# Optimization experiments

Measured on AMD Instinct MI355X. Metric: run time of the kernel, lower is better.

## Reference

```python
import jax, jax.numpy as jnp
import numpy as np
import math

B, NPG, DEG = 100, 500, 12          # graphs, nodes/graph, avg degree
F_IN, H, C = 128, 128, 10
RATIO = 0.5
N = B * NPG
E = N * DEG
K1 = math.ceil(NPG * RATIO)          # 250
K2 = math.ceil(K1 * RATIO)           # 125
K3 = math.ceil(K2 * RATIO)           # 63


def _lin(k, i, o):
    return jax.random.uniform(k, (i, o), jnp.float32, -1.0, 1.0) / np.sqrt(i).astype(np.float32)


def setup_inputs() -> dict:
    key = jax.random.key(0)
    ks = jax.random.split(key, 16)
    x = jax.random.normal(ks[0], (N, F_IN), jnp.float32)
    off = (jnp.arange(B, dtype=jnp.int32) * NPG)[:, None]
    src = (jax.random.randint(ks[1], (B, NPG * DEG), 0, NPG, jnp.int32) + off).reshape(-1)
    dst = (jax.random.randint(ks[2], (B, NPG * DEG), 0, NPG, jnp.int32) + off).reshape(-1)
    edge_index = jnp.stack([src, dst])
    return {
        'x': x, 'edge_index': edge_index,
        'Wl1': _lin(ks[3], F_IN, H), 'bl1': jnp.zeros((H,), jnp.float32), 'Wr1': _lin(ks[4], F_IN, H),
        'Wl2': _lin(ks[5], H, H), 'bl2': jnp.zeros((H,), jnp.float32), 'Wr2': _lin(ks[6], H, H),
        'Wl3': _lin(ks[7], H, H), 'bl3': jnp.zeros((H,), jnp.float32), 'Wr3': _lin(ks[8], H, H),
        'pw1': jax.random.normal(ks[9], (H,), jnp.float32),
        'pw2': jax.random.normal(ks[10], (H,), jnp.float32),
        'pw3': jax.random.normal(ks[11], (H,), jnp.float32),
        'W1': _lin(ks[12], 2 * H, H), 'b1': jnp.zeros((H,), jnp.float32),
        'W2': _lin(ks[13], H, H // 2), 'b2': jnp.zeros((H // 2,), jnp.float32),
        'W3': _lin(ks[14], H // 2, C), 'b3': jnp.zeros((C,), jnp.float32),
    }


def sage_conv(x, src, dst, emask, Wl, bl, Wr, n_nodes):
    # PyG SAGEConv: out_i = lin_l(mean_{j->i} x_j) + lin_r(x_i)
    msg = x[src] * emask[:, None]                                   # [E, d]
    agg = jax.ops.segment_sum(msg, dst, num_segments=n_nodes)
    cnt = jax.ops.segment_sum(emask, dst, num_segments=n_nodes)
    mean = agg / jnp.maximum(cnt, 1.0)[:, None]
    return mean @ Wl + bl + x @ Wr


def topk_pool(x, w, src, dst, emask, n_per, k):
    # TopKPooling: score = tanh(x.w/||w||); keep top-k nodes per graph; x_kept *= score
    score = jnp.tanh((x @ w) / jnp.linalg.norm(w))                  # [B*n_per]
    topv, topi = jax.lax.top_k(score.reshape(B, n_per), k)          # [B, k]
    perm = (topi + (jnp.arange(B, dtype=jnp.int32) * n_per)[:, None]).reshape(-1)
    x_new = x[perm] * topv.reshape(-1)[:, None]                     # [B*k, d]
    mapping = jnp.full((B * n_per,), -1, jnp.int32).at[perm].set(jnp.arange(B * k, dtype=jnp.int32))
    ns, nd = mapping[src], mapping[dst]
    emask_new = emask * ((ns >= 0) & (nd >= 0)).astype(emask.dtype)
    return x_new, jnp.maximum(ns, 0), jnp.maximum(nd, 0), emask_new


def readout(x, k):
    # global_max_pool || global_mean_pool (all graphs have exactly k nodes)
    xr = x.reshape(B, k, H)
    return jnp.concatenate([xr.max(axis=1), xr.mean(axis=1)], axis=1)  # [B, 2H]


def reference(x, edge_index, Wl1, bl1, Wr1, Wl2, bl2, Wr2, Wl3, bl3, Wr3,
              pw1, pw2, pw3, W1, b1, W2, b2, W3, b3):
    src, dst = edge_index[0], edge_index[1]
    emask = jnp.ones((E,), jnp.float32)
    h = jax.nn.relu(sage_conv(x, src, dst, emask, Wl1, bl1, Wr1, N))
    h, src, dst, emask = topk_pool(h, pw1, src, dst, emask, NPG, K1)
    x1 = readout(h, K1)
    h = jax.nn.relu(sage_conv(h, src, dst, emask, Wl2, bl2, Wr2, B * K1))
    h, src, dst, emask = topk_pool(h, pw2, src, dst, emask, K1, K2)
    x2 = readout(h, K2)
    h = jax.nn.relu(sage_conv(h, src, dst, emask, Wl3, bl3, Wr3, B * K2))
    h, src, dst, emask = topk_pool(h, pw3, src, dst, emask, K2, K3)
    x3 = readout(h, K3)
    z = x1 + x2 + x3
    z = jax.nn.relu(z @ W1 + b1)   # dropout is identity in eval mode
    z = jax.nn.relu(z @ W2 + b2)
    return jax.nn.log_softmax(z @ W3 + b3, axis=1)   # pool_loss == 0 for TopKPool
```

## Files before the change

kernel.cpp:

```cpp
#include <hip/hip_runtime.h>
#include <math.h>

#define BG    100
#define NPG   500
#define FD    128
#define EE    600000
#define EPG   6000
#define NN    50000
#define K1    250
#define K2    125
#define K3    63
#define CAP   64

typedef short v8s __attribute__((ext_vector_type(8)));
typedef float v4f __attribute__((ext_vector_type(4)));

__device__ __forceinline__ int swz(int p, int N) {
    int j = p & 7, i = p >> 3;
    int chunk = N >> 3, rem = N & 7;
    int mj = j < rem ? j : rem;
    return j * chunk + mj + i;
}

__device__ __forceinline__ unsigned short f2bf(float f) {
    unsigned int u = __float_as_uint(f);
    unsigned int r = (u + 0x7FFFu + ((u >> 16) & 1u)) >> 16;
    return (unsigned short)r;
}
__device__ __forceinline__ float bf2f(unsigned short b) {
    return __uint_as_float(((unsigned int)b) << 16);
}

__global__ __launch_bounds__(1024) void prep_fill_kernel(
        const int* __restrict__ ei, int* __restrict__ deg, int* __restrict__ col,
        const float* __restrict__ Wl1, const float* __restrict__ Wr1,
        const float* __restrict__ Wl2, const float* __restrict__ Wr2,
        const float* __restrict__ Wl3, const float* __restrict__ Wr3,
        unsigned short* __restrict__ wt_hi, unsigned short* __restrict__ wt_lo) {
    __shared__ int lcnt[NPG];
    int tid = threadIdx.x;
    if (blockIdx.x < BG) {
        int b = swz(blockIdx.x, BG);
        for (int i = tid; i < NPG; i += 1024) lcnt[i] = 0;
        __syncthreads();
        for (int e0 = tid; e0 < EPG; e0 += 1024) {
            int e = b * EPG + e0;
            int d = ei[EE + e];
            int pos = atomicAdd(&lcnt[d - b * NPG], 1);
            if (pos < CAP) col[(long long)d * CAP + pos] = ei[e];
        }
        __syncthreads();
        for (int i = tid; i < NPG; i += 1024) deg[b * NPG + i] = lcnt[i];
    } else {
        int id = (blockIdx.x - BG) * 1024 + tid;
        if (id >= 3 * 256 * 128) return;
        int layer = id >> 15, rem = id & 32767;
        int k = rem >> 7, n = rem & 127;
        const float* Wl = layer == 0 ? Wl1 : (layer == 1 ? Wl2 : Wl3);
        const float* Wr = layer == 0 ? Wr1 : (layer == 1 ? Wr2 : Wr3);
        float w = (k < 128) ? Wl[k * 128 + n] : Wr[(k - 128) * 128 + n];
        unsigned short hi = f2bf(w);
        unsigned short lo = f2bf(w - bf2f(hi));
        long long o = (long long)layer * 32768 + n * 256 + k;
        wt_hi[o] = hi;
        wt_lo[o] = lo;
    }
}

__global__ void gather_agg_kernel(const int* __restrict__ deg, const int* __restrict__ col,
                                  const float* __restrict__ x, float* __restrict__ mean,
                                  int n, int NB) {
    int g = swz(blockIdx.x, NB) * 256 + threadIdx.x;
    int node = g >> 5, sub = g & 31;
    if (node >= n) return;
    int d = deg[node]; if (d > CAP) d = CAP;
    const int* cp = col + (long long)node * CAP;
    float ax = 0.0f, ay = 0.0f, az = 0.0f, aw = 0.0f;
    int j = 0;
    for (; j + 4 <= d; j += 4) {
        int s0 = cp[j], s1 = cp[j + 1], s2 = cp[j + 2], s3 = cp[j + 3];
        float4 v0 = ((const float4*)(x + (long long)s0 * FD))[sub];
        float4 v1 = ((const float4*)(x + (long long)s1 * FD))[sub];
        float4 v2 = ((const float4*)(x + (long long)s2 * FD))[sub];
        float4 v3 = ((const float4*)(x + (long long)s3 * FD))[sub];
        ax += v0.x; ay += v0.y; az += v0.z; aw += v0.w;
        ax += v1.x; ay += v1.y; az += v1.z; aw += v1.w;
        ax += v2.x; ay += v2.y; az += v2.z; aw += v2.w;
        ax += v3.x; ay += v3.y; az += v3.z; aw += v3.w;
    }
    for (; j < d; ++j) {
        float4 v = ((const float4*)(x + (long long)cp[j] * FD))[sub];
        ax += v.x; ay += v.y; az += v.z; aw += v.w;
    }
    float inv = 1.0f / fmaxf((float)d, 1.0f);
    float4 o; o.x = ax * inv; o.y = ay * inv; o.z = az * inv; o.w = aw * inv;
    ((float4*)(mean + (long long)node * FD))[sub] = o;
}

__global__ __launch_bounds__(256) void sage_gemm_mfma_kernel(
        const float* __restrict__ mean, const float* __restrict__ x,
        const unsigned short* __restrict__ wt_hi, const unsigned short* __restrict__ wt_lo,
        const float* __restrict__ bl, const float* __restrict__ pw,
        float* __restrict__ hout, float* __restrict__ score, int M, int NB) {
    __shared__ unsigned short Bh[128 * 40], Bl[128 * 40];
    __shared__ float spart[64 * 16];
    __shared__ float snrmp[16];
    int tid  = threadIdx.x;
    int wave = tid >> 6, lane = tid & 63;
    int quad = lane >> 4, l15 = lane & 15;
    int row0 = swz(blockIdx.x, NB) * 64;

    v4f acc[8];
#pragma unroll
    for (int t = 0; t < 8; t++) acc[t] = (v4f){0.f, 0.f, 0.f, 0.f};

    if (tid < 16) {
        float s = 0.f;
#pragma unroll
        for (int t = 0; t < 8; t++) { float p = pw[t * 16 + tid]; s += p * p; }
        snrmp[tid] = s;
    }

    int growA = row0 + 16 * wave + l15; if (growA > M - 1) growA = M - 1;
    int brow = tid >> 1;
    int bk   = (tid & 1) * 16;

    for (int kt = 0; kt < 8; ++kt) {
        const float* Ab = (kt < 4) ? mean : x;
        const float* ap = Ab + (long long)growA * FD + ((kt < 4) ? kt : kt - 4) * 32 + quad * 8;
        float4 v0 = *(const float4*)(ap);
        float4 v1 = *(const float4*)(ap + 4);
        {
            int klog = kt * 32;
            const uint4* sh = (const uint4*)(wt_hi + (long long)brow * 256 + klog + bk);
            const uint4* sl = (const uint4*)(wt_lo + (long long)brow * 256 + klog + bk);
            uint4 vh0 = sh[0], vh1 = sh[1];
            uint4 vl0 = sl[0], vl1 = sl[1];
            *(uint4*)&Bh[brow * 40 + bk]     = vh0;
            *(uint4*)&Bh[brow * 40 + bk + 8] = vh1;
            *(uint4*)&Bl[brow * 40 + bk]     = vl0;
            *(uint4*)&Bl[brow * 40 + bk + 8] = vl1;
        }
        float f[8] = {v0.x, v0.y, v0.z, v0.w, v1.x, v1.y, v1.z, v1.w};
        v8s a_h, a_l;
#pragma unroll
        for (int q = 0; q < 8; q++) {
            unsigned short hb = f2bf(f[q]);
            a_h[q] = (short)hb;
            a_l[q] = (short)f2bf(f[q] - bf2f(hb));
        }
        __syncthreads();
#pragma unroll
        for (int t = 0; t < 8; t++) {
            v8s b_h = *(const v8s*)&Bh[(t * 16 + l15) * 40 + quad * 8];
            v8s b_l = *(const v8s*)&Bl[(t * 16 + l15) * 40 + quad * 8];
            acc[t] = __builtin_amdgcn_mfma_f32_16x16x32_bf16(a_l, b_h, acc[t], 0, 0, 0);
            acc[t] = __builtin_amdgcn_mfma_f32_16x16x32_bf16(a_h, b_l, acc[t], 0, 0, 0);
            acc[t] = __builtin_amdgcn_mfma_f32_16x16x32_bf16(a_h, b_h, acc[t], 0, 0, 0);
        }
        __syncthreads();
    }

    int rbase = row0 + 16 * wave + quad * 4;
    float part[4] = {0.f, 0.f, 0.f, 0.f};
#pragma unroll
    for (int t = 0; t < 8; t++) {
        int colc = t * 16 + l15;
        float blv = bl[colc];
        float pwv = pw[colc];
#pragma unroll
        for (int reg = 0; reg < 4; reg++) {
            float h = fmaxf(acc[t][reg] + blv, 0.0f);
            part[reg] += h * pwv;
            int grow = rbase + reg;
            if (grow < M) hout[(long long)grow * FD + colc] = h;
        }
    }
#pragma unroll
    for (int reg = 0; reg < 4; reg++)
        spart[(16 * wave + quad * 4 + reg) * 16 + l15] = part[reg];
    __syncthreads();
    if (tid < 64) {
        int grow = row0 + tid;
        if (grow < M) {
            float dot = 0.0f;
#pragma unroll
            for (int i = 0; i < 16; i++) dot += spart[tid * 16 + i];
            float nr = 0.0f;
#pragma unroll
            for (int i = 0; i < 16; i++) nr += snrmp[i];
            score[grow] = tanhf(dot / sqrtf(nr));
        }
    }
}

__global__ __launch_bounds__(1024) void topk_tail_kernel(
        const float* __restrict__ score, const float* __restrict__ hout,
        int n_per, int k, int SN,
        float* __restrict__ xp,
        const int* __restrict__ esrc, const int* __restrict__ edst,
        const float* __restrict__ em_in,
        int* __restrict__ src_out, int* __restrict__ dst_out, float* __restrict__ em_out,
        int* __restrict__ next_deg, int* __restrict__ next_col,
        float* __restrict__ z, int mode,
        const float* __restrict__ W1, const float* __restrict__ b1,
        const float* __restrict__ W2, const float* __restrict__ b2,
        const float* __restrict__ W3, const float* __restrict__ b3,
        float* __restrict__ out) {
    __shared__ float skey[512];
    __shared__ int   sidx[512];
    __shared__ unsigned long long spk[512];
    __shared__ int   lmap[512];
    __shared__ int   lcnt[512];
    __shared__ float pmax[1024];
    __shared__ float psum[1024];
    __shared__ float zs[256], t1[128], t2[64], t3[16];
    int b = swz(blockIdx.x, BG), tid = threadIdx.x;

    for (int i = tid; i < SN; i += 1024) { lmap[i] = -1; lcnt[i] = 0; }

    unsigned long long P = 0ULL;
    if (tid < SN) {
        float keyv; unsigned int idx;
        if (tid < n_per) { keyv = score[b * n_per + tid]; idx = (unsigned int)tid; }
        else             { keyv = -INFINITY;              idx = 0x7fffffffu; }
        unsigned int u = __float_as_uint(keyv);
        u = (u & 0x80000000u) ? ~u : (u | 0x80000000u);
        P = ((unsigned long long)u << 32) | (unsigned long long)(~idx);
    }

    for (int ks = 2; ks <= SN; ks <<= 1) {
        for (int j = ks >> 1; j > 0; j >>= 1) {
            unsigned long long Q;
            if (j >= 64) {
                __syncthreads();
                if (tid < SN) spk[tid] = P;
                __syncthreads();
                Q = (tid < SN) ? spk[tid ^ j] : 0ULL;
            } else {
                Q = __shfl_xor(P, j, 64);
            }
            if (tid < SN) {
                bool keepmax = (((tid & ks) == 0) == ((tid & j) == 0));
                if (keepmax == (Q > P)) P = Q;
            }
        }
    }
    if (tid < SN) {
        unsigned int u  = (unsigned int)(P >> 32);
        unsigned int fb = (u & 0x80000000u) ? (u & 0x7fffffffu) : ~u;
        int iv = (int)(~(unsigned int)P);
        skey[tid] = __uint_as_float(fb);
        sidx[tid] = iv;
        if (tid < k) lmap[iv] = tid;
    }
    __syncthreads();

    if (esrc) {
        int nbase = b * n_per, kbase = b * k;
        for (int e0 = tid; e0 < EPG; e0 += 1024) {
            int e = b * EPG + e0;
            bool alive = em_in ? (em_in[e] != 0.0f) : true;
            if (alive) {
                int ls = lmap[esrc[e] - nbase];
                int ld = lmap[edst[e] - nbase];
                bool keep = (ls >= 0) && (ld >= 0);
                if (keep) {
                    int pos = atomicAdd(&lcnt[ld], 1);
                    if (pos < CAP) next_col[(long long)(kbase + ld) * CAP + pos] = kbase + ls;
                }
                if (em_out) {
                    em_out[e]  = keep ? 1.0f : 0.0f;
                    src_out[e] = keep ? kbase + ls : 0;
                    dst_out[e] = keep ? kbase + ld : 0;
                }
            } else if (em_out) {
                em_out[e] = 0.0f; src_out[e] = 0; dst_out[e] = 0;
            }
        }
        __syncthreads();
        for (int i = tid; i < k; i += 1024) next_deg[b * k + i] = lcnt[i];
    }

    int c = tid & 127, s = tid >> 7;
    float mx = -INFINITY, sm = 0.0f;
    {
        int r = s;
        long long hbase = (long long)b * n_per * FD + c;
        long long xbase = (long long)b * k * FD + c;
        for (; r + 24 < k; r += 32) {
            int i0 = sidx[r], i1 = sidx[r + 8], i2 = sidx[r + 16], i3 = sidx[r + 24];
            float k0 = skey[r], k1 = skey[r + 8], k2 = skey[r + 16], k3 = skey[r + 24];
            float v0 = hout[hbase + (long long)i0 * FD] * k0;
            float v1 = hout[hbase + (long long)i1 * FD] * k1;
            float v2 = hout[hbase + (long long)i2 * FD] * k2;
            float v3 = hout[hbase + (long long)i3 * FD] * k3;
            xp[xbase + (long long)(r)      * FD] = v0;
            xp[xbase + (long long)(r + 8)  * FD] = v1;
            xp[xbase + (long long)(r + 16) * FD] = v2;
            xp[xbase + (long long)(r + 24) * FD] = v3;
            mx = fmaxf(mx, v0); sm += v0;
            mx = fmaxf(mx, v1); sm += v1;
            mx = fmaxf(mx, v2); sm += v2;
            mx = fmaxf(mx, v3); sm += v3;
        }
        for (; r < k; r += 8) {
            float v = hout[hbase + (long long)sidx[r] * FD] * skey[r];
            xp[xbase + (long long)r * FD] = v;
            mx = fmaxf(mx, v); sm += v;
        }
    }
    pmax[tid] = mx; psum[tid] = sm;
    __syncthreads();
    if (tid < 128) {
        float m = -INFINITY, su = 0.0f;
#pragma unroll
        for (int i = 0; i < 8; i++) {
            m = fmaxf(m, pmax[i * 128 + tid]);
            su += psum[i * 128 + tid];
        }
        float mean = su / (float)k;
        if (mode == 0)      { z[b * 256 + tid] = m;  z[b * 256 + 128 + tid] = mean;  }
        else if (mode == 1) { z[b * 256 + tid] += m; z[b * 256 + 128 + tid] += mean; }
        else {
            zs[tid]       = z[b * 256 + tid] + m;
            zs[128 + tid] = z[b * 256 + 128 + tid] + mean;
        }
    }
    if (mode == 2) {
        __syncthreads();
        if (tid < 128) {
            float a = b1[tid];
            for (int kk = 0; kk < 256; kk++) a += zs[kk] * W1[kk * 128 + tid];
            t1[tid] = fmaxf(a, 0.0f);
        }
        __syncthreads();
        if (tid < 64) {
            float a = b2[tid];
            for (int kk = 0; kk < 128; kk++) a += t1[kk] * W2[kk * 64 + tid];
            t2[tid] = fmaxf(a, 0.0f);
        }
        __syncthreads();
        if (tid < 10) {
            float a = b3[tid];
            for (int kk = 0; kk < 64; kk++) a += t2[kk] * W3[kk * 10 + tid];
            t3[tid] = a;
        }
        __syncthreads();
        if (tid == 0) {
            float m = -INFINITY;
            for (int i = 0; i < 10; i++) m = fmaxf(m, t3[i]);
            float su = 0.0f;
            for (int i = 0; i < 10; i++) su += expf(t3[i] - m);
            float ls = logf(su);
            for (int i = 0; i < 10; i++) out[b * 10 + i] = t3[i] - m - ls;
        }
    }
}

extern "C" void kernel_launch(void* const* d_in, const int* in_sizes, int n_in,
                              void* d_out, int out_size, void* d_ws, size_t ws_size,
                              hipStream_t stream) {
    (void)in_sizes; (void)n_in; (void)out_size; (void)ws_size;
    const float* x   = (const float*)d_in[0];
    const int*   ei  = (const int*)d_in[1];
    const float* Wl1 = (const float*)d_in[2];
    const float* bl1 = (const float*)d_in[3];
    const float* Wr1 = (const float*)d_in[4];
    const float* Wl2 = (const float*)d_in[5];
    const float* bl2 = (const float*)d_in[6];
    const float* Wr2 = (const float*)d_in[7];
    const float* Wl3 = (const float*)d_in[8];
    const float* bl3 = (const float*)d_in[9];
    const float* Wr3 = (const float*)d_in[10];
    const float* pw1 = (const float*)d_in[11];
    const float* pw2 = (const float*)d_in[12];
    const float* pw3 = (const float*)d_in[13];
    const float* W1  = (const float*)d_in[14];
    const float* b1  = (const float*)d_in[15];
    const float* W2  = (const float*)d_in[16];
    const float* b2  = (const float*)d_in[17];
    const float* W3  = (const float*)d_in[18];
    const float* b3  = (const float*)d_in[19];
    float* out = (float*)d_out;

    char* ws = (char*)d_ws;
    size_t off = 0;
    auto alloc = [&](size_t bytes) {
        char* p = ws + off;
        off = (off + bytes + 255) & ~(size_t)255;
        return p;
    };
    float* mean  = (float*)alloc((size_t)NN * FD * 4);
    float* hout  = (float*)alloc((size_t)NN * FD * 4);
    float* xp    = (float*)alloc((size_t)BG * K1 * FD * 4);
    float* sc    = (float*)alloc((size_t)NN * 4);
    int*   srcb  = (int*)  alloc((size_t)EE * 4);
    int*   dstb  = (int*)  alloc((size_t)EE * 4);
    float* emb   = (float*)alloc((size_t)EE * 4);
    int*   deg   = (int*)  alloc((size_t)NN * 4);
    int*   colb  = (int*)  alloc((size_t)NN * CAP * 4);
    float* z     = (float*)alloc((size_t)BG * 256 * 4);
    unsigned short* wt_hi = (unsigned short*)alloc((size_t)3 * 32768 * 2);
    unsigned short* wt_lo = (unsigned short*)alloc((size_t)3 * 32768 * 2);

    prep_fill_kernel<<<BG + 96, 1024, 0, stream>>>(ei, deg, colb,
                                                   Wl1, Wr1, Wl2, Wr2, Wl3, Wr3, wt_hi, wt_lo);

    {
        int nb = (NN * 32 + 255) / 256;
        gather_agg_kernel<<<nb, 256, 0, stream>>>(deg, colb, x, mean, NN, nb);
    }
    {
        int nb = (NN + 63) / 64;
        sage_gemm_mfma_kernel<<<nb, 256, 0, stream>>>(mean, x, wt_hi, wt_lo,
                                                      bl1, pw1, hout, sc, NN, nb);
    }
    topk_tail_kernel<<<BG, 1024, 0, stream>>>(sc, hout, NPG, K1, 512, xp,
                                              ei, ei + EE, (const float*)0,
                                              srcb, dstb, emb, deg, colb,
                                              z, 0, W1, b1, W2, b2, W3, b3, out);

    const int N2 = BG * K1;
    {
        int nb = (N2 * 32 + 255) / 256;
        gather_agg_kernel<<<nb, 256, 0, stream>>>(deg, colb, xp, mean, N2, nb);
    }
    {
        int nb = (N2 + 63) / 64;
        sage_gemm_mfma_kernel<<<nb, 256, 0, stream>>>(mean, xp, wt_hi + 32768, wt_lo + 32768,
                                                      bl2, pw2, hout, sc, N2, nb);
    }
    topk_tail_kernel<<<BG, 1024, 0, stream>>>(sc, hout, K1, K2, 256, xp,
                                              srcb, dstb, emb,
                                              (int*)0, (int*)0, (float*)0, deg, colb,
                                              z, 1, W1, b1, W2, b2, W3, b3, out);

    const int N3 = BG * K2;
    {
        int nb = (N3 * 32 + 255) / 256;
        gather_agg_kernel<<<nb, 256, 0, stream>>>(deg, colb, xp, mean, N3, nb);
    }
    {
        int nb = (N3 + 63) / 64;
        sage_gemm_mfma_kernel<<<nb, 256, 0, stream>>>(mean, xp, wt_hi + 65536, wt_lo + 65536,
                                                      bl3, pw3, hout, sc, N3, nb);
    }
    topk_tail_kernel<<<BG, 1024, 0, stream>>>(sc, hout, K2, K3, 128, xp,
                                              (const int*)0, (const int*)0, (const float*)0,
                                              (int*)0, (int*)0, (float*)0, (int*)0, (int*)0,
                                              z, 2, W1, b1, W2, b2, W3, b3, out);
}
```

Measured before the change: 261.2 us.

## Fuse mean-neighbour aggregation for pooled layers into topk tail kernel

The topk_tail kernel now computes the mean aggregation over kept neighbours right after pooling, using its shared-memory degree counts and the freshly written xp rows. This removes two gather_agg launches and the next_deg round trip through global memory. It also skips writing xp in the final pooling stage, where xp is no longer read. The trade-off is that aggregation runs on only 100 blocks instead of a wide grid, so it may use the GPU less fully. The fused gather also relies on xp writes from the same block being visible after __syncthreads, which holds because every edge is intra-graph.

```diff
diff --git a/kernel.cpp b/kernel.cpp
--- a/kernel.cpp
+++ b/kernel.cpp
@@ -201,7 +201,7 @@
         const int* __restrict__ esrc, const int* __restrict__ edst,
         const float* __restrict__ em_in,
         int* __restrict__ src_out, int* __restrict__ dst_out, float* __restrict__ em_out,
-        int* __restrict__ next_deg, int* __restrict__ next_col,
+        int* __restrict__ next_col, float* __restrict__ mean_out,
         float* __restrict__ z, int mode,
         const float* __restrict__ W1, const float* __restrict__ b1,
         const float* __restrict__ W2, const float* __restrict__ b2,
@@ -278,9 +278,8 @@
                 em_out[e] = 0.0f; src_out[e] = 0; dst_out[e] = 0;
             }
         }
-        __syncthreads();
-        for (int i = tid; i < k; i += 1024) next_deg[b * k + i] = lcnt[i];
-    }
+    }
+    __syncthreads();
 
     int c = tid & 127, s = tid >> 7;
     float mx = -INFINITY, sm = 0.0f;
@@ -295,10 +294,12 @@
             float v1 = hout[hbase + (long long)i1 * FD] * k1;
             float v2 = hout[hbase + (long long)i2 * FD] * k2;
             float v3 = hout[hbase + (long long)i3 * FD] * k3;
-            xp[xbase + (long long)(r)      * FD] = v0;
-            xp[xbase + (long long)(r + 8)  * FD] = v1;
-            xp[xbase + (long long)(r + 16) * FD] = v2;
-            xp[xbase + (long long)(r + 24) * FD] = v3;
+            if (mode != 2) {
+                xp[xbase + (long long)(r)      * FD] = v0;
+                xp[xbase + (long long)(r + 8)  * FD] = v1;
+                xp[xbase + (long long)(r + 16) * FD] = v2;
+                xp[xbase + (long long)(r + 24) * FD] = v3;
+            }
             mx = fmaxf(mx, v0); sm += v0;
             mx = fmaxf(mx, v1); sm += v1;
             mx = fmaxf(mx, v2); sm += v2;
@@ -306,7 +307,7 @@
         }
         for (; r < k; r += 8) {
             float v = hout[hbase + (long long)sidx[r] * FD] * skey[r];
-            xp[xbase + (long long)r * FD] = v;
+            if (mode != 2) xp[xbase + (long long)r * FD] = v;
             mx = fmaxf(mx, v); sm += v;
         }
     }
@@ -327,6 +328,7 @@
             zs[128 + tid] = z[b * 256 + 128 + tid] + mean;
         }
     }
+
     if (mode == 2) {
         __syncthreads();
         if (tid < 128) {
@@ -354,6 +356,37 @@
             for (int i = 0; i < 10; i++) su += expf(t3[i] - m);
             float ls = logf(su);
             for (int i = 0; i < 10; i++) out[b * 10 + i] = t3[i] - m - ls;
+        }
+        return;
+    }
+
+    if (mean_out) {
+        __syncthreads();
+        int grp = tid >> 5, sub = tid & 31;
+        int kbase = b * k;
+        for (int node = grp; node < k; node += 32) {
+            int d = lcnt[node]; if (d > CAP) d = CAP;
+            const int* cp = next_col + (long long)(kbase + node) * CAP;
+            float ax = 0.0f, ay = 0.0f, az = 0.0f, aw = 0.0f;
+            int j = 0;
+            for (; j + 4 <= d; j += 4) {
+                int s0 = cp[j], s1 = cp[j + 1], s2 = cp[j + 2], s3 = cp[j + 3];
+                float4 v0 = ((const float4*)(xp + (long long)s0 * FD))[sub];
+                float4 v1 = ((const float4*)(xp + (long long)s1 * FD))[sub];
+                float4 v2 = ((const float4*)(xp + (long long)s2 * FD))[sub];
+                float4 v3 = ((const float4*)(xp + (long long)s3 * FD))[sub];
+                ax += v0.x; ay += v0.y; az += v0.z; aw += v0.w;
+                ax += v1.x; ay += v1.y; az += v1.z; aw += v1.w;
+                ax += v2.x; ay += v2.y; az += v2.z; aw += v2.w;
+                ax += v3.x; ay += v3.y; az += v3.z; aw += v3.w;
+            }
+            for (; j < d; ++j) {
+                float4 v = ((const float4*)(xp + (long long)cp[j] * FD))[sub];
+                ax += v.x; ay += v.y; az += v.z; aw += v.w;
+            }
+            float inv = 1.0f / fmaxf((float)d, 1.0f);
+            float4 o; o.x = ax * inv; o.y = ay * inv; o.z = az * inv; o.w = aw * inv;
+            ((float4*)(mean_out + (long long)(kbase + node) * FD))[sub] = o;
         }
     }
 }
@@ -418,14 +451,10 @@
     }
     topk_tail_kernel<<<BG, 1024, 0, stream>>>(sc, hout, NPG, K1, 512, xp,
                                               ei, ei + EE, (const float*)0,
-                                              srcb, dstb, emb, deg, colb,
+                                              srcb, dstb, emb, colb, mean,
                                               z, 0, W1, b1, W2, b2, W3, b3, out);
 
     const int N2 = BG * K1;
-    {
-        int nb = (N2 * 32 + 255) / 256;
-        gather_agg_kernel<<<nb, 256, 0, stream>>>(deg, colb, xp, mean, N2, nb);
-    }
     {
         int nb = (N2 + 63) / 64;
         sage_gemm_mfma_kernel<<<nb, 256, 0, stream>>>(mean, xp, wt_hi + 32768, wt_lo + 32768,
@@ -433,21 +462,17 @@
     }
     topk_tail_kernel<<<BG, 1024, 0, stream>>>(sc, hout, K1, K2, 256, xp,
                                               srcb, dstb, emb,
-                                              (int*)0, (int*)0, (float*)0, deg, colb,
+                                              (int*)0, (int*)0, (float*)0, colb, mean,
                                               z, 1, W1, b1, W2, b2, W3, b3, out);
 
     const int N3 = BG * K2;
-    {
-        int nb = (N3 * 32 + 255) / 256;
-        gather_agg_kernel<<<nb, 256, 0, stream>>>(deg, colb, xp, mean, N3, nb);
-    }
     {
         int nb = (N3 + 63) / 64;
         sage_gemm_mfma_kernel<<<nb, 256, 0, stream>>>(mean, xp, wt_hi + 65536, wt_lo + 65536,
                                                       bl3, pw3, hout, sc, N3, nb);
     }
-    topk_tail_kernel<<<BG, 1024, 0, stream>>>(sc, hout, K2, K3, 128, xp,
+    topk_tail_kernel<<<BG, 1024, 0, stream>>>(sc, hout, K2, K3, 128, (float*)0,
                                               (const int*)0, (const int*)0, (const float*)0,
-                                              (int*)0, (int*)0, (float*)0, (int*)0, (int*)0,
+                                              (int*)0, (int*)0, (float*)0, (int*)0, (float*)0,
                                               z, 2, W1, b1, W2, b2, W3, b3, out);
 }
```

Result: slower. 268.7 us (+2.9%).

## Split topk tail into edge-remap and feature blocks, replace edge arrays with node map

Applied to the files above, without the earlier changes.

The top-k tail kernel now launches twice as many blocks. One half rebuilds the pooled adjacency and the other half does feature gathering and readout, so the two jobs run concurrently instead of serially in one block. The per-edge src/dst/mask output arrays are replaced by a per-node global map, which cuts edge-sized writes. The second pooling level re-derives kept edges from the original edge list through the map. The last level also skips writing pooled features nobody reads. Both halves redo the bitonic sort, so sort work is duplicated in exchange.

```diff
diff --git a/kernel.cpp b/kernel.cpp
--- a/kernel.cpp
+++ b/kernel.cpp
@@ -199,8 +199,7 @@
         int n_per, int k, int SN,
         float* __restrict__ xp,
         const int* __restrict__ esrc, const int* __restrict__ edst,
-        const float* __restrict__ em_in,
-        int* __restrict__ src_out, int* __restrict__ dst_out, float* __restrict__ em_out,
+        int* __restrict__ gmap,
         int* __restrict__ next_deg, int* __restrict__ next_col,
         float* __restrict__ z, int mode,
         const float* __restrict__ W1, const float* __restrict__ b1,
@@ -215,7 +214,13 @@
     __shared__ float pmax[1024];
     __shared__ float psum[1024];
     __shared__ float zs[256], t1[128], t2[64], t3[16];
-    int b = swz(blockIdx.x, BG), tid = threadIdx.x;
+    int tid = threadIdx.x;
+    int kind, b;
+    if (mode == 2) { kind = 1; b = swz(blockIdx.x, BG); }
+    else {
+        kind = blockIdx.x >= BG ? 1 : 0;
+        b = swz(kind ? blockIdx.x - BG : blockIdx.x, BG);
+    }
 
     for (int i = tid; i < SN; i += 1024) { lmap[i] = -1; lcnt[i] = 0; }
 
@@ -228,7 +233,6 @@
         u = (u & 0x80000000u) ? ~u : (u | 0x80000000u);
         P = ((unsigned long long)u << 32) | (unsigned long long)(~idx);
     }
-
     for (int ks = 2; ks <= SN; ks <<= 1) {
         for (int j = ks >> 1; j > 0; j >>= 1) {
             unsigned long long Q;
@@ -256,30 +260,41 @@
     }
     __syncthreads();
 
-    if (esrc) {
-        int nbase = b * n_per, kbase = b * k;
-        for (int e0 = tid; e0 < EPG; e0 += 1024) {
-            int e = b * EPG + e0;
-            bool alive = em_in ? (em_in[e] != 0.0f) : true;
-            if (alive) {
+    if (kind == 0) {
+        int kbase = b * k;
+        if (mode == 0) {
+            int nbase = b * n_per;
+            for (int e0 = tid; e0 < EPG; e0 += 1024) {
+                int e = b * EPG + e0;
                 int ls = lmap[esrc[e] - nbase];
                 int ld = lmap[edst[e] - nbase];
-                bool keep = (ls >= 0) && (ld >= 0);
-                if (keep) {
+                if (ls >= 0 && ld >= 0) {
                     int pos = atomicAdd(&lcnt[ld], 1);
                     if (pos < CAP) next_col[(long long)(kbase + ld) * CAP + pos] = kbase + ls;
                 }
-                if (em_out) {
-                    em_out[e]  = keep ? 1.0f : 0.0f;
-                    src_out[e] = keep ? kbase + ls : 0;
-                    dst_out[e] = keep ? kbase + ld : 0;
+            }
+            __syncthreads();
+            for (int i = tid; i < NPG; i += 1024) {
+                int l = lmap[i];
+                gmap[nbase + i] = l >= 0 ? kbase + l : -1;
+            }
+        } else {
+            int kb1 = b * n_per;
+            for (int e0 = tid; e0 < EPG; e0 += 1024) {
+                int e = b * EPG + e0;
+                int ws = gmap[esrc[e]];
+                int wd = gmap[edst[e]];
+                int ls = (ws >= 0) ? lmap[ws - kb1] : -1;
+                int ld = (wd >= 0) ? lmap[wd - kb1] : -1;
+                if (ls >= 0 && ld >= 0) {
+                    int pos = atomicAdd(&lcnt[ld], 1);
+                    if (pos < CAP) next_col[(long long)(kbase + ld) * CAP + pos] = kbase + ls;
                 }
-            } else if (em_out) {
-                em_out[e] = 0.0f; src_out[e] = 0; dst_out[e] = 0;
-            }
-        }
-        __syncthreads();
-        for (int i = tid; i < k; i += 1024) next_deg[b * k + i] = lcnt[i];
+            }
+            __syncthreads();
+        }
+        for (int i = tid; i < k; i += 1024) next_deg[kbase + i] = lcnt[i];
+        return;
     }
 
     int c = tid & 127, s = tid >> 7;
@@ -295,10 +310,12 @@
             float v1 = hout[hbase + (long long)i1 * FD] * k1;
             float v2 = hout[hbase + (long long)i2 * FD] * k2;
             float v3 = hout[hbase + (long long)i3 * FD] * k3;
-            xp[xbase + (long long)(r)      * FD] = v0;
-            xp[xbase + (long long)(r + 8)  * FD] = v1;
-            xp[xbase + (long long)(r + 16) * FD] = v2;
-            xp[xbase + (long long)(r + 24) * FD] = v3;
+            if (mode != 2) {
+                xp[xbase + (long long)(r)      * FD] = v0;
+                xp[xbase + (long long)(r + 8)  * FD] = v1;
+                xp[xbase + (long long)(r + 16) * FD] = v2;
+                xp[xbase + (long long)(r + 24) * FD] = v3;
+            }
             mx = fmaxf(mx, v0); sm += v0;
             mx = fmaxf(mx, v1); sm += v1;
             mx = fmaxf(mx, v2); sm += v2;
@@ -306,7 +323,7 @@
         }
         for (; r < k; r += 8) {
             float v = hout[hbase + (long long)sidx[r] * FD] * skey[r];
-            xp[xbase + (long long)r * FD] = v;
+            if (mode != 2) xp[xbase + (long long)r * FD] = v;
             mx = fmaxf(mx, v); sm += v;
         }
     }
@@ -395,9 +412,7 @@
     float* hout  = (float*)alloc((size_t)NN * FD * 4);
     float* xp    = (float*)alloc((size_t)BG * K1 * FD * 4);
     float* sc    = (float*)alloc((size_t)NN * 4);
-    int*   srcb  = (int*)  alloc((size_t)EE * 4);
-    int*   dstb  = (int*)  alloc((size_t)EE * 4);
-    float* emb   = (float*)alloc((size_t)EE * 4);
+    int*   gmap  = (int*)  alloc((size_t)NN * 4);
     int*   deg   = (int*)  alloc((size_t)NN * 4);
     int*   colb  = (int*)  alloc((size_t)NN * CAP * 4);
     float* z     = (float*)alloc((size_t)BG * 256 * 4);
@@ -416,10 +431,9 @@
         sage_gemm_mfma_kernel<<<nb, 256, 0, stream>>>(mean, x, wt_hi, wt_lo,
                                                       bl1, pw1, hout, sc, NN, nb);
     }
-    topk_tail_kernel<<<BG, 1024, 0, stream>>>(sc, hout, NPG, K1, 512, xp,
-                                              ei, ei + EE, (const float*)0,
-                                              srcb, dstb, emb, deg, colb,
-                                              z, 0, W1, b1, W2, b2, W3, b3, out);
+    topk_tail_kernel<<<2 * BG, 1024, 0, stream>>>(sc, hout, NPG, K1, 512, xp,
+                                                  ei, ei + EE, gmap, deg, colb,
+                                                  z, 0, W1, b1, W2, b2, W3, b3, out);
 
     const int N2 = BG * K1;
     {
@@ -431,10 +445,9 @@
         sage_gemm_mfma_kernel<<<nb, 256, 0, stream>>>(mean, xp, wt_hi + 32768, wt_lo + 32768,
                                                       bl2, pw2, hout, sc, N2, nb);
     }
-    topk_tail_kernel<<<BG, 1024, 0, stream>>>(sc, hout, K1, K2, 256, xp,
-                                              srcb, dstb, emb,
-                                              (int*)0, (int*)0, (float*)0, deg, colb,
-                                              z, 1, W1, b1, W2, b2, W3, b3, out);
+    topk_tail_kernel<<<2 * BG, 1024, 0, stream>>>(sc, hout, K1, K2, 256, xp,
+                                                  ei, ei + EE, gmap, deg, colb,
+                                                  z, 1, W1, b1, W2, b2, W3, b3, out);
 
     const int N3 = BG * K2;
     {
@@ -446,8 +459,8 @@
         sage_gemm_mfma_kernel<<<nb, 256, 0, stream>>>(mean, xp, wt_hi + 65536, wt_lo + 65536,
                                                       bl3, pw3, hout, sc, N3, nb);
     }
-    topk_tail_kernel<<<BG, 1024, 0, stream>>>(sc, hout, K2, K3, 128, xp,
-                                              (const int*)0, (const int*)0, (const float*)0,
-                                              (int*)0, (int*)0, (float*)0, (int*)0, (int*)0,
+    topk_tail_kernel<<<BG, 1024, 0, stream>>>(sc, hout, K2, K3, 128, (float*)0,
+                                              (const int*)0, (const int*)0, (int*)0,
+                                              (int*)0, (int*)0,
                                               z, 2, W1, b1, W2, b2, W3, b3, out);
 }
```

New measurement: 256.2 us. No clear change (-1.9%).
